# Performance work log

Hardware: AMD Instinct MI355X
Metric: run time of the kernel (lower is better)

The kernel has to match this reference:

```python
import jax, jax.numpy as jnp
import numpy as np

DIM = 384
HEADS = 8
SR = 2
EPS = 1e-5


def setup_inputs() -> dict:
    key = jax.random.key(0)
    ks = jax.random.split(key, 10)
    B, H, W, C = 16, 56, 56, DIM
    s = 0.02
    return {
        "x": jax.random.normal(ks[0], (B, H * W, C), jnp.float32),
        "qkv_w": jax.random.normal(ks[1], (3 * C, C), jnp.float32) * s,
        "qkv_b": jnp.zeros((3 * C,), jnp.float32),
        "proj_w": jax.random.normal(ks[2], (C, C), jnp.float32) * s,
        "proj_b": jnp.zeros((C,), jnp.float32),
        "lp_w": jax.random.normal(ks[3], (C, SR, SR), jnp.float32) * s,  # depthwise convT weight (C,1,sr,sr) squeezed
        "lp_b": jnp.zeros((C,), jnp.float32),
        "ln_w": jnp.ones((C,), jnp.float32),
        "ln_b": jnp.zeros((C,), jnp.float32),
        "H": 56,
        "W": 56,
    }


def reference(x, qkv_w, qkv_b, proj_w, proj_b, lp_w, lp_b, ln_w, ln_b, H, W):
    B, N, C = x.shape
    hd = C // HEADS
    scale = hd ** -0.5

    # AvgPool2d(kernel=(1,1), stride=(sr,sr)) == strided subsampling
    xi = x.transpose(0, 2, 1).reshape(B, C, H, W)[:, :, ::SR, ::SR]
    h, w = H // SR, W // SR
    n = h * w
    xs = xi.reshape(B, C, n).transpose(0, 2, 1)  # [B, n, C]

    qkv = (xs @ qkv_w.T + qkv_b).reshape(B, n, 3, HEADS, hd).transpose(2, 0, 3, 1, 4)
    q, k, v = qkv[0], qkv[1], qkv[2]  # each [B, heads, n, hd]

    attn = jax.nn.softmax(jnp.einsum('bhqd,bhkd->bhqk', q, k) * scale, axis=-1)
    o = jnp.einsum('bhqk,bhkd->bhqd', attn, v).transpose(0, 2, 1, 3).reshape(B, n, C)

    # ConvTranspose2d(C, C, kernel=sr, stride=sr, groups=C): each input pixel
    # expands to an sr x sr block scaled by the per-channel kernel.
    oi = o.transpose(0, 2, 1).reshape(B, C, h, w)
    up = jnp.einsum('bchw,cpq->bchpwq', oi, lp_w).reshape(B, C, H, W)
    up = up + lp_b[None, :, None, None]

    y = up.reshape(B, C, N).transpose(0, 2, 1)  # [B, N, C]
    mu = y.mean(-1, keepdims=True)
    var = y.var(-1, keepdims=True)
    y = (y - mu) * jax.lax.rsqrt(var + EPS) * ln_w + ln_b

    return y @ proj_w.T + proj_b
```

## Files before the change

### kernel.cpp

```cpp
#include <hip/hip_runtime.h>
#include <math.h>

#define CDIM 384
#define NHEADS 8
#define HD 48
#define NQ 784
#define NQPAD 832
#define NB 16
#define HWD 56
#define NPIX 3136
#define QK_SCALE (0.14433756729740643f * 1.4426950408889634f)
#define LN_EPS 1e-5f
#define WSCALE 16.0f
#define WUNSCALE 0.0625f

typedef _Float16 f16;
typedef _Float16 f16x4 __attribute__((ext_vector_type(4)));
typedef _Float16 f16x8 __attribute__((ext_vector_type(8)));
typedef float f32x4 __attribute__((ext_vector_type(4)));

__device__ __forceinline__ float waveSum(float v) {
#pragma unroll
  for (int o = 32; o > 0; o >>= 1) v += __shfl_xor(v, o);
  return v;
}

__device__ __forceinline__ float fast_exp2(float x) {
#if __has_builtin(__builtin_amdgcn_exp2f)
  return __builtin_amdgcn_exp2f(x);
#else
  return __expf(x * 0.6931471805599453f);
#endif
}

__device__ __forceinline__ void gload16(const void* g, void* l) {
  __builtin_amdgcn_global_load_lds(
      (const __attribute__((address_space(1))) void*)g,
      (__attribute__((address_space(3))) void*)l, 16, 0, 0);
}

__device__ __forceinline__ int xcd_chunk_lin(int b, int nwg) {
  const int c = b & 7, s = b >> 3;
  const int q = nwg >> 3, r = nwg & 7;
  const int off = (c < r) ? c * (q + 1) : r * (q + 1) + (c - r) * q;
  return off + s;
}

__global__ __launch_bounds__(256) void prep_kernel(
    const float* __restrict__ x, f16* __restrict__ xp,
    const float* __restrict__ qkv_w, f16* __restrict__ qkv_wh,
    f16* __restrict__ vt, const float* __restrict__ pw,
    const float* __restrict__ lpw, const float* __restrict__ lnw,
    const float* __restrict__ lp_b, const float* __restrict__ ln_b,
    const float* __restrict__ pb, f16* __restrict__ wq,
    float* __restrict__ cvec) {
  const int blk = blockIdx.x, t = threadIdx.x;
  if (blk < 4704) {
    const int i = (blk * 256 + t) * 4;
    const int row = i / CDIM, col = i % CDIM;
    const int b = row / NQ, qi = row % NQ;
    const int hi = qi / 28, wi = qi % 28;
    const float4 v =
        *(const float4*)(x + ((size_t)(b * NPIX + hi * 112 + wi * 2)) * CDIM + col);
    f16x4 h;
    h.x = (f16)v.x; h.y = (f16)v.y; h.z = (f16)v.z; h.w = (f16)v.w;
    *(f16x4*)(xp + i) = h;
  } else if (blk < 5136) {
    const int i = ((blk - 4704) * 256 + t) * 4;
    const float4 v = *(const float4*)(qkv_w + i);
    f16x4 h;
    h.x = (f16)v.x; h.y = (f16)v.y; h.z = (f16)v.z; h.w = (f16)v.w;
    *(f16x4*)(qkv_wh + i) = h;
  } else if (blk < 5280) {
    const int idx = (blk - 5136) * 256 + t;
    const int row = idx / 6, off = idx % 6;
    float4* p = (float4*)vt + (size_t)row * 104 + 98 + off;
    *p = make_float4(0.f, 0.f, 0.f, 0.f);
  } else if (blk < 5856) {
    const int i4 = ((blk - 5280) * 256 + t) * 4;
    const int f = i4 / CDIM, c = i4 % CDIM;
    const int pq = f / CDIM, j = f % CDIM;
    const float4 wv = *(const float4*)(pw + (size_t)j * CDIM + c);
    const float4 ln = *(const float4*)(lnw + c);
    f16x4 h;
    h.x = (f16)(wv.x * lpw[(c + 0) * 4 + pq] * ln.x * WSCALE);
    h.y = (f16)(wv.y * lpw[(c + 1) * 4 + pq] * ln.y * WSCALE);
    h.z = (f16)(wv.z * lpw[(c + 2) * 4 + pq] * ln.z * WSCALE);
    h.w = (f16)(wv.w * lpw[(c + 3) * 4 + pq] * ln.w * WSCALE);
    *(f16x4*)(wq + i4) = h;
  } else {
    const int j = (blk - 5856) * 4 + (t >> 6);
    const int lane = t & 63;
    float a1 = 0.f, a2 = 0.f, a3 = 0.f;
#pragma unroll
    for (int i = 0; i < 6; ++i) {
      const int c = lane + i * 64;
      const float wv = pw[(size_t)j * CDIM + c];
      a1 += lp_b[c] * lnw[c] * wv;
      a2 += lnw[c] * wv;
      a3 += ln_b[c] * wv;
    }
    a1 = waveSum(a1);
    a2 = waveSum(a2);
    a3 = waveSum(a3);
    if (lane == 0) {
      cvec[j] = a1;
      cvec[CDIM + j] = a2;
      cvec[2 * CDIM + j] = a3 + pb[j];
    }
  }
}

__device__ __forceinline__ void mfma_tile_gemm_db(
    const f16* __restrict__ A, const f16* __restrict__ B, int m0, int n0,
    int K, f32x4 (&acc)[4][4], f16* As, f16* Bs) {
  const int t = threadIdx.x;
  const int lane = t & 63, w = t >> 6;
  const int wm = w >> 1, wn = w & 1;
  const int l15 = lane & 15, l4 = lane >> 4;
  const int rowS = t >> 2;
  const int kb = (t & 3) * 16;
  char* AsB = (char*)As;
  char* BsB = (char*)Bs;
  const char* Ag = (const char*)A + ((size_t)(m0 + rowS) * K) * 2 + kb;
  const char* Bg = (const char*)B + ((size_t)(n0 + rowS) * K) * 2 + kb;
  const size_t row64 = (size_t)64 * K * 2;

  gload16(Ag, AsB + t * 16);
  gload16(Ag + row64, AsB + 4096 + t * 16);
  gload16(Bg, BsB + t * 16);
  gload16(Bg + row64, BsB + 4096 + t * 16);

  int cur = 0;
  for (int k0 = 0; k0 < K; k0 += 32) {
    __syncthreads();
    if (k0 + 32 < K) {
      const int nb_ = cur ^ 1;
      const char* Ag2 = Ag + (size_t)(k0 + 32) * 2;
      const char* Bg2 = Bg + (size_t)(k0 + 32) * 2;
      gload16(Ag2, AsB + nb_ * 8192 + t * 16);
      gload16(Ag2 + row64, AsB + nb_ * 8192 + 4096 + t * 16);
      gload16(Bg2, BsB + nb_ * 8192 + t * 16);
      gload16(Bg2 + row64, BsB + nb_ * 8192 + 4096 + t * 16);
    }
    const char* Ab = AsB + cur * 8192;
    const char* Bb = BsB + cur * 8192;
    f16x8 af[4], bf[4];
#pragma unroll
    for (int i = 0; i < 4; ++i)
      af[i] = *(const f16x8*)(Ab + ((wm * 64 + i * 16 + l15) * 64 + l4 * 16));
#pragma unroll
    for (int j = 0; j < 4; ++j)
      bf[j] = *(const f16x8*)(Bb + ((wn * 64 + j * 16 + l15) * 64 + l4 * 16));
#pragma unroll
    for (int i = 0; i < 4; ++i)
#pragma unroll
      for (int j = 0; j < 4; ++j)
        acc[i][j] =
            __builtin_amdgcn_mfma_f32_16x16x32_f16(af[i], bf[j], acc[i][j], 0, 0, 0);
    cur ^= 1;
  }
}

__global__ __launch_bounds__(256) void qkv_mfma_kernel(
    const f16* __restrict__ xp, const f16* __restrict__ wh,
    const float* __restrict__ qkv_b, f16* __restrict__ qh,
    f16* __restrict__ kh, f16* __restrict__ vt) {
  __shared__ union SU {
    struct { f16 As[2 * 128 * 32]; f16 Bs[2 * 128 * 32]; } s;
    f16 Tr[128][136];
  } u;
  const int lin = xcd_chunk_lin(blockIdx.x, 882);
  const int m0 = (lin / 9) * 128, n0 = (lin % 9) * 128;
  f32x4 acc[4][4] = {};
  mfma_tile_gemm_db(xp, wh, m0, n0, CDIM, acc, u.s.As, u.s.Bs);

  const int t = threadIdx.x, lane = t & 63, w = t >> 6;
  const int wm = w >> 1, wn = w & 1;
  const int l15 = lane & 15, l4 = lane >> 4;
  const int sec = n0 / CDIM;
  const float scl = (sec == 0) ? QK_SCALE : 1.f;

  __syncthreads();

  if (sec < 2) {
#pragma unroll
    for (int j = 0; j < 4; ++j) {
      const int fl_ = wn * 64 + j * 16 + l15;
      const float bias = qkv_b[n0 + fl_];
#pragma unroll
      for (int i = 0; i < 4; ++i)
#pragma unroll
        for (int r = 0; r < 4; ++r)
          u.Tr[wm * 64 + i * 16 + l4 * 4 + r][fl_] =
              (f16)((acc[i][j][r] + bias) * scl);
    }
  } else {
#pragma unroll
    for (int j = 0; j < 4; ++j) {
      const int fl_ = wn * 64 + j * 16 + l15;
      const float bias = qkv_b[n0 + fl_];
#pragma unroll
      for (int i = 0; i < 4; ++i)
#pragma unroll
        for (int r = 0; r < 4; ++r)
          u.Tr[fl_][wm * 64 + i * 16 + l4 * 4 + r] = (f16)(acc[i][j][r] + bias);
    }
  }
  __syncthreads();

#pragma unroll
  for (int c = 0; c < 8; ++c) {
    const int v = c * 256 + t;
    const int rr = v >> 4, u16 = v & 15;
    if (sec < 2) {
      const int qi_l = rr, f_l = u16 * 8;
      const int fr = n0 + f_l - sec * CDIM;
      const int hh = fr / HD, d = fr - hh * HD;
      const int mm = m0 + qi_l, b = mm / NQ, tok = mm - b * NQ;
      f16* dst = (sec == 0 ? qh : kh) +
                 ((size_t)(b * NHEADS + hh) * NQ + tok) * HD + d;
      *(f16x8*)dst = *(const f16x8*)&u.Tr[qi_l][f_l];
    } else {
      const int f_l = rr, qi0 = u16 * 8;
      const int fr = n0 + f_l - 2 * CDIM;
      const int hh = fr / HD, d = fr - hh * HD;
      const int mm = m0 + qi0, b = mm / NQ, tok = mm - b * NQ;
      f16* dst = vt + ((size_t)(b * NHEADS + hh) * HD + d) * NQPAD + tok;
      *(f16x8*)dst = *(const f16x8*)&u.Tr[f_l][qi0];
    }
  }
}

__global__ __launch_bounds__(256) void flash_kernel(
    const f16* __restrict__ qh, const f16* __restrict__ kh,
    const f16* __restrict__ vt, f16* __restrict__ o16) {
  __shared__ f16 PQ[128 * 72];
  __shared__ f16 Ks[64][64];
  __shared__ f16 Vts[48][64];

  f16 (*Qs)[72] = (f16(*)[72])PQ;
  f16 (*Ps)[32][68] = (f16(*)[32][68])PQ;

  const int t = threadIdx.x;
  const int lane = t & 63, w = t >> 6;
  const int quad = lane >> 4, l15 = lane & 15;
  const int q0 = blockIdx.x * 128;
  const int bh = blockIdx.y;

  const f16* qg = qh + (size_t)bh * NQ * HD;
  const f16* kg = kh + (size_t)bh * NQ * HD;
  const f16* vg = vt + (size_t)bh * HD * NQPAD;

  {
    const f16x8 z8 = {};
    *(f16x8*)&Qs[t >> 1][48 + (t & 1) * 8] = z8;
    if (t < 128) {
      const int row = t >> 1, zc = 6 + (t & 1);
      *(f16x8*)&Ks[row][(zc ^ (row & 7)) * 8] = z8;
    }
  }

#pragma unroll
  for (int c = 0; c < 3; ++c) {
    const int u = t + c * 256;
    const int row = u / 6, seg = u % 6;
    const int gr = min(q0 + row, NQ - 1);
    *(f16x8*)&Qs[row][seg * 8] =
        *(const f16x8*)(qg + (size_t)gr * HD + seg * 8);
  }
  __syncthreads();

  f16x8 qf0[2], qf1[2];
#pragma unroll
  for (int qa = 0; qa < 2; ++qa) {
    const int row = w * 32 + qa * 16 + l15;
    qf0[qa] = *(const f16x8*)&Qs[row][quad * 8];
    qf1[qa] = *(const f16x8*)&Qs[row][32 + quad * 8];
  }

  const f16* gp[3];
  f16* lp[3];
  int step[3];
#pragma unroll
  for (int c = 0; c < 3; ++c) {
    const int u = t + c * 256;
    if (u < 384) {
      const int row = u / 6, seg = u % 6;
      gp[c] = kg + (size_t)row * HD + seg * 8;
      lp[c] = &Ks[row][(seg ^ (row & 7)) * 8];
      step[c] = 64 * HD;
    } else {
      const int uv = u - 384;
      const int row = uv >> 3, seg = uv & 7;
      gp[c] = vg + (size_t)row * NQPAD + seg * 8;
      lp[c] = &Vts[row][(seg ^ (row & 7)) * 8];
      step[c] = 64;
    }
  }

  f16x8 rg[3];
#pragma unroll
  for (int c = 0; c < 3; ++c) {
    rg[c] = *(const f16x8*)gp[c];
    gp[c] += step[c];
  }

  f32x4 accO[2][3] = {};
  float l_[2][4] = {};

  for (int kt = 0; kt < 13; ++kt) {
#pragma unroll
    for (int c = 0; c < 3; ++c) *(f16x8*)lp[c] = rg[c];
    __syncthreads();
    if (kt < 12) {
#pragma unroll
      for (int c = 0; c < 3; ++c) {
        rg[c] = *(const f16x8*)gp[c];
        gp[c] += step[c];
      }
    }

    const bool last = (kt == 12);
#pragma unroll
    for (int j = 0; j < 4; ++j) {
      const int krow = j * 16 + l15, ksw = krow & 7;
      const f16x8 b0 = *(const f16x8*)&Ks[krow][(quad ^ ksw) * 8];
      const f16x8 b1 = *(const f16x8*)&Ks[krow][((4 + quad) ^ ksw) * 8];
      f32x4 z0 = {}, z1 = {};
      z0 = __builtin_amdgcn_mfma_f32_16x16x32_f16(qf0[0], b0, z0, 0, 0, 0);
      const f32x4 sj0 = __builtin_amdgcn_mfma_f32_16x16x32_f16(qf1[0], b1, z0, 0, 0, 0);
      z1 = __builtin_amdgcn_mfma_f32_16x16x32_f16(qf0[1], b0, z1, 0, 0, 0);
      const f32x4 sj1 = __builtin_amdgcn_mfma_f32_16x16x32_f16(qf1[1], b1, z1, 0, 0, 0);
      const bool msk = last && (j >= 1);
#pragma unroll
      for (int r = 0; r < 4; ++r) {
        const float p0 = msk ? 0.f : fast_exp2(sj0[r]);
        const float p1 = msk ? 0.f : fast_exp2(sj1[r]);
        l_[0][r] += p0;
        l_[1][r] += p1;
        Ps[w][quad * 4 + r][j * 16 + l15] = (f16)p0;
        Ps[w][16 + quad * 4 + r][j * 16 + l15] = (f16)p1;
      }
    }

    f16x8 ap0[2], ap1[2];
#pragma unroll
    for (int qa = 0; qa < 2; ++qa) {
      const int row = qa * 16 + l15;
      const f16x4 a0 = *(const f16x4*)&Ps[w][row][quad * 8];
      const f16x4 a1 = *(const f16x4*)&Ps[w][row][quad * 8 + 4];
      const f16x4 a2 = *(const f16x4*)&Ps[w][row][32 + quad * 8];
      const f16x4 a3 = *(const f16x4*)&Ps[w][row][32 + quad * 8 + 4];
      ap0[qa] = __builtin_shufflevector(a0, a1, 0, 1, 2, 3, 4, 5, 6, 7);
      ap1[qa] = __builtin_shufflevector(a2, a3, 0, 1, 2, 3, 4, 5, 6, 7);
    }

#pragma unroll
    for (int jn = 0; jn < 3; ++jn) {
      const int vrow = jn * 16 + l15, vsw = vrow & 7;
      const f16x8 v0 = *(const f16x8*)&Vts[vrow][(quad ^ vsw) * 8];
      const f16x8 v1 = *(const f16x8*)&Vts[vrow][((4 + quad) ^ vsw) * 8];
#pragma unroll
      for (int qa = 0; qa < 2; ++qa) {
        accO[qa][jn] =
            __builtin_amdgcn_mfma_f32_16x16x32_f16(ap0[qa], v0, accO[qa][jn], 0, 0, 0);
        accO[qa][jn] =
            __builtin_amdgcn_mfma_f32_16x16x32_f16(ap1[qa], v1, accO[qa][jn], 0, 0, 0);
      }
    }
    __syncthreads();
  }

  const int b = bh >> 3, hh = bh & 7;
#pragma unroll
  for (int qa = 0; qa < 2; ++qa) {
#pragma unroll
    for (int r = 0; r < 4; ++r) {
      float rs = l_[qa][r];
      rs += __shfl_xor(rs, 1);
      rs += __shfl_xor(rs, 2);
      rs += __shfl_xor(rs, 4);
      rs += __shfl_xor(rs, 8);
      const int qrow = q0 + w * 32 + qa * 16 + quad * 4 + r;
      if (qrow < NQ) {
        const float inv = 1.f / rs;
#pragma unroll
        for (int jn = 0; jn < 3; ++jn)
          o16[((size_t)(b * NQ + qrow)) * CDIM + hh * HD + jn * 16 + l15] =
              (f16)(accO[qa][jn][r] * inv);
      }
    }
  }
}

__global__ __launch_bounds__(256) void stats_kernel(
    const f16* __restrict__ o16, const float* __restrict__ lp_w,
    const float* __restrict__ lp_b, float* __restrict__ stats) {
  const int m = blockIdx.x * 4 + (threadIdx.x >> 6);
  const int lane = threadIdx.x & 63;
  float s[4] = {}, ss[4] = {};
#pragma unroll
  for (int i = 0; i < 6; ++i) {
    const int c = lane + i * 64;
    const float ov = (float)o16[(size_t)m * CDIM + c];
    const float4 w4 = *(const float4*)(lp_w + c * 4);
    const float bb = lp_b[c];
    const float u0 = ov * w4.x + bb;
    const float u1 = ov * w4.y + bb;
    const float u2 = ov * w4.z + bb;
    const float u3 = ov * w4.w + bb;
    s[0] += u0; ss[0] += u0 * u0;
    s[1] += u1; ss[1] += u1 * u1;
    s[2] += u2; ss[2] += u2 * u2;
    s[3] += u3; ss[3] += u3 * u3;
  }
#pragma unroll
  for (int pq = 0; pq < 4; ++pq) {
    s[pq] = waveSum(s[pq]);
    ss[pq] = waveSum(ss[pq]);
  }
  if (lane < 4) {
    const float mu = s[lane] * (1.f / CDIM);
    const float var = ss[lane] * (1.f / CDIM) - mu * mu;
    stats[m * 8 + lane * 2] = mu;
    stats[m * 8 + lane * 2 + 1] = rsqrtf(var + LN_EPS);
  }
}

__global__ __launch_bounds__(256) void projfused_kernel(
    const f16* __restrict__ o16, const f16* __restrict__ wq,
    const float* __restrict__ stats, const float* __restrict__ cvec,
    float* __restrict__ out) {
  __shared__ f16 As[2 * 128 * 32];
  __shared__ f16 Bs[2 * 128 * 32];
  const int lin = xcd_chunk_lin(blockIdx.x, 1176);
  const int m0 = (lin / 12) * 128, n0 = (lin % 12) * 128;
  f32x4 acc[4][4] = {};
  mfma_tile_gemm_db(o16, wq, m0, n0, CDIM, acc, As, Bs);

  const int t = threadIdx.x, lane = t & 63, w = t >> 6;
  const int wm = w >> 1, wn = w & 1;
  const int l15 = lane & 15, l4 = lane >> 4;
  const int pq = n0 / CDIM;
  const int p = pq >> 1, q = pq & 1;
  const int c0 = n0 - pq * CDIM;

  float C1[4], C2[4], C3[4];
#pragma unroll
  for (int j = 0; j < 4; ++j) {
    const int col = c0 + wn * 64 + j * 16 + l15;
    C1[j] = cvec[col];
    C2[j] = cvec[CDIM + col];
    C3[j] = cvec[2 * CDIM + col];
  }

#pragma unroll
  for (int i = 0; i < 4; ++i) {
#pragma unroll
    for (int r = 0; r < 4; ++r) {
      const int m = m0 + wm * 64 + i * 16 + l4 * 4 + r;
      const int b = m / NQ, n = m % NQ;
      const int hi2 = n / 28, wi2 = n % 28;
      const float mu = stats[m * 8 + pq * 2];
      const float rstd = stats[m * 8 + pq * 2 + 1];
      const int pix = (hi2 * 2 + p) * HWD + (wi2 * 2 + q);
      float* orow = out + ((size_t)(b * NPIX + pix)) * CDIM;
#pragma unroll
      for (int j = 0; j < 4; ++j) {
        const int col = c0 + wn * 64 + j * 16 + l15;
        orow[col] = rstd * (acc[i][j][r] * WUNSCALE + C1[j] - mu * C2[j]) + C3[j];
      }
    }
  }
}

extern "C" void kernel_launch(void* const* d_in, const int* in_sizes, int n_in,
                              void* d_out, int out_size, void* d_ws,
                              size_t ws_size, hipStream_t stream) {
  const float* x      = (const float*)d_in[0];
  const float* qkv_w  = (const float*)d_in[1];
  const float* qkv_b  = (const float*)d_in[2];
  const float* proj_w = (const float*)d_in[3];
  const float* proj_b = (const float*)d_in[4];
  const float* lp_w   = (const float*)d_in[5];
  const float* lp_b   = (const float*)d_in[6];
  const float* ln_w   = (const float*)d_in[7];
  const float* ln_b   = (const float*)d_in[8];
  float* out = (float*)d_out;

  float* ws = (float*)d_ws;
  f16* o16 = (f16*)ws;
  float* zreg = ws + 2408448;
  f16* qh = (f16*)zreg;
  f16* kh = qh + (size_t)128 * NQ * HD;
  f16* vt = kh + (size_t)128 * NQ * HD;
  float* rest = zreg + 7372800;
  f16* xp = (f16*)rest;
  f16* qkv_wh = xp + (size_t)12544 * CDIM;
  float* rest2 = rest + 2408448 + 221184;
  f16* wq = (f16*)rest2;
  float* cvec = rest2 + 1179648;
  float* stats = cvec + 1152;

  prep_kernel<<<dim3(5952), 256, 0, stream>>>(x, xp, qkv_w, qkv_wh, vt, proj_w,
                                              lp_w, ln_w, lp_b, ln_b, proj_b,
                                              wq, cvec);

  qkv_mfma_kernel<<<dim3(882), 256, 0, stream>>>(xp, qkv_wh, qkv_b, qh, kh, vt);

  flash_kernel<<<dim3(7, 128), 256, 0, stream>>>(qh, kh, vt, o16);

  stats_kernel<<<dim3(3136), 256, 0, stream>>>(o16, lp_w, lp_b, stats);

  projfused_kernel<<<dim3(1176), 256, 0, stream>>>(o16, wq, stats, cvec, out);
}
```

Before: 242.8 us.

## Triple-buffer GEMM LDS pipeline with explicit vmcnt waits; pad flash K/V tiles

The shared GEMM mainloop moves from a double-buffered scheme with a full __syncthreads per step to a three-stage LDS ring. Two K-slices are kept in flight, and explicit s_waitcnt vmcnt plus a raw s_barrier replace the full synchronisation, aiming to hide global-load latency behind the MFMA work. K is fixed to CDIM and the loop is fully unrolled. In the flash kernel the XOR-swizzled K/V LDS tiles become row-padded (stride 72) tiles, which simplifies addressing but costs more LDS. The larger LDS footprint in the GEMM kernels may reduce occupancy.

```diff
diff --git a/kernel.cpp b/kernel.cpp
--- a/kernel.cpp
+++ b/kernel.cpp
@@ -111,9 +111,9 @@
   }
 }
 
-__device__ __forceinline__ void mfma_tile_gemm_db(
+__device__ __forceinline__ void mfma_tile_gemm_pipe(
     const f16* __restrict__ A, const f16* __restrict__ B, int m0, int n0,
-    int K, f32x4 (&acc)[4][4], f16* As, f16* Bs) {
+    f32x4 (&acc)[4][4], f16* As, f16* Bs) {
   const int t = threadIdx.x;
   const int lane = t & 63, w = t >> 6;
   const int wm = w >> 1, wn = w & 1;
@@ -122,29 +122,35 @@
   const int kb = (t & 3) * 16;
   char* AsB = (char*)As;
   char* BsB = (char*)Bs;
-  const char* Ag = (const char*)A + ((size_t)(m0 + rowS) * K) * 2 + kb;
-  const char* Bg = (const char*)B + ((size_t)(n0 + rowS) * K) * 2 + kb;
-  const size_t row64 = (size_t)64 * K * 2;
-
-  gload16(Ag, AsB + t * 16);
-  gload16(Ag + row64, AsB + 4096 + t * 16);
-  gload16(Bg, BsB + t * 16);
-  gload16(Bg + row64, BsB + 4096 + t * 16);
-
-  int cur = 0;
-  for (int k0 = 0; k0 < K; k0 += 32) {
-    __syncthreads();
-    if (k0 + 32 < K) {
-      const int nb_ = cur ^ 1;
-      const char* Ag2 = Ag + (size_t)(k0 + 32) * 2;
-      const char* Bg2 = Bg + (size_t)(k0 + 32) * 2;
-      gload16(Ag2, AsB + nb_ * 8192 + t * 16);
-      gload16(Ag2 + row64, AsB + nb_ * 8192 + 4096 + t * 16);
-      gload16(Bg2, BsB + nb_ * 8192 + t * 16);
-      gload16(Bg2 + row64, BsB + nb_ * 8192 + 4096 + t * 16);
-    }
-    const char* Ab = AsB + cur * 8192;
-    const char* Bb = BsB + cur * 8192;
+  const char* Ag = (const char*)A + ((size_t)(m0 + rowS) * CDIM) * 2 + kb;
+  const char* Bg = (const char*)B + ((size_t)(n0 + rowS) * CDIM) * 2 + kb;
+  const size_t row64 = (size_t)64 * CDIM * 2;
+
+#define ISSUE(kk)                                           \
+  do {                                                      \
+    const int bofs = ((kk) % 3) * 8192;                     \
+    const char* Ag2 = Ag + (size_t)(kk) * 64;               \
+    const char* Bg2 = Bg + (size_t)(kk) * 64;               \
+    gload16(Ag2, AsB + bofs + t * 16);                      \
+    gload16(Ag2 + row64, AsB + bofs + 4096 + t * 16);       \
+    gload16(Bg2, BsB + bofs + t * 16);                      \
+    gload16(Bg2 + row64, BsB + bofs + 4096 + t * 16);       \
+  } while (0)
+
+  ISSUE(0);
+  ISSUE(1);
+
+#pragma unroll
+  for (int k = 0; k < 12; ++k) {
+    if (k < 11)
+      asm volatile("s_waitcnt vmcnt(4)" ::: "memory");
+    else
+      asm volatile("s_waitcnt vmcnt(0)" ::: "memory");
+    __builtin_amdgcn_s_barrier();
+    __builtin_amdgcn_sched_barrier(0);
+    if (k + 2 < 12) ISSUE(k + 2);
+    const char* Ab = AsB + (k % 3) * 8192;
+    const char* Bb = BsB + (k % 3) * 8192;
     f16x8 af[4], bf[4];
 #pragma unroll
     for (int i = 0; i < 4; ++i)
@@ -158,8 +164,8 @@
       for (int j = 0; j < 4; ++j)
         acc[i][j] =
             __builtin_amdgcn_mfma_f32_16x16x32_f16(af[i], bf[j], acc[i][j], 0, 0, 0);
-    cur ^= 1;
-  }
+  }
+#undef ISSUE
 }
 
 __global__ __launch_bounds__(256) void qkv_mfma_kernel(
@@ -167,13 +173,13 @@
     const float* __restrict__ qkv_b, f16* __restrict__ qh,
     f16* __restrict__ kh, f16* __restrict__ vt) {
   __shared__ union SU {
-    struct { f16 As[2 * 128 * 32]; f16 Bs[2 * 128 * 32]; } s;
+    struct { f16 As[3 * 128 * 32]; f16 Bs[3 * 128 * 32]; } s;
     f16 Tr[128][136];
   } u;
   const int lin = xcd_chunk_lin(blockIdx.x, 882);
   const int m0 = (lin / 9) * 128, n0 = (lin % 9) * 128;
   f32x4 acc[4][4] = {};
-  mfma_tile_gemm_db(xp, wh, m0, n0, CDIM, acc, u.s.As, u.s.Bs);
+  mfma_tile_gemm_pipe(xp, wh, m0, n0, acc, u.s.As, u.s.Bs);
 
   const int t = threadIdx.x, lane = t & 63, w = t >> 6;
   const int wm = w >> 1, wn = w & 1;
@@ -236,8 +242,8 @@
     const f16* __restrict__ qh, const f16* __restrict__ kh,
     const f16* __restrict__ vt, f16* __restrict__ o16) {
   __shared__ f16 PQ[128 * 72];
-  __shared__ f16 Ks[64][64];
-  __shared__ f16 Vts[48][64];
+  __shared__ f16 Ks[64][72];
+  __shared__ f16 Vts[48][72];
 
   f16 (*Qs)[72] = (f16(*)[72])PQ;
   f16 (*Ps)[32][68] = (f16(*)[32][68])PQ;
@@ -255,10 +261,7 @@
   {
     const f16x8 z8 = {};
     *(f16x8*)&Qs[t >> 1][48 + (t & 1) * 8] = z8;
-    if (t < 128) {
-      const int row = t >> 1, zc = 6 + (t & 1);
-      *(f16x8*)&Ks[row][(zc ^ (row & 7)) * 8] = z8;
-    }
+    if (t < 128) *(f16x8*)&Ks[t >> 1][48 + (t & 1) * 8] = z8;
   }
 
 #pragma unroll
@@ -288,13 +291,13 @@
     if (u < 384) {
       const int row = u / 6, seg = u % 6;
       gp[c] = kg + (size_t)row * HD + seg * 8;
-      lp[c] = &Ks[row][(seg ^ (row & 7)) * 8];
+      lp[c] = &Ks[row][seg * 8];
       step[c] = 64 * HD;
     } else {
       const int uv = u - 384;
       const int row = uv >> 3, seg = uv & 7;
       gp[c] = vg + (size_t)row * NQPAD + seg * 8;
-      lp[c] = &Vts[row][(seg ^ (row & 7)) * 8];
+      lp[c] = &Vts[row][seg * 8];
       step[c] = 64;
     }
   }
@@ -324,9 +327,8 @@
     const bool last = (kt == 12);
 #pragma unroll
     for (int j = 0; j < 4; ++j) {
-      const int krow = j * 16 + l15, ksw = krow & 7;
-      const f16x8 b0 = *(const f16x8*)&Ks[krow][(quad ^ ksw) * 8];
-      const f16x8 b1 = *(const f16x8*)&Ks[krow][((4 + quad) ^ ksw) * 8];
+      const f16x8 b0 = *(const f16x8*)&Ks[j * 16 + l15][quad * 8];
+      const f16x8 b1 = *(const f16x8*)&Ks[j * 16 + l15][32 + quad * 8];
       f32x4 z0 = {}, z1 = {};
       z0 = __builtin_amdgcn_mfma_f32_16x16x32_f16(qf0[0], b0, z0, 0, 0, 0);
       const f32x4 sj0 = __builtin_amdgcn_mfma_f32_16x16x32_f16(qf1[0], b1, z0, 0, 0, 0);
@@ -358,9 +360,8 @@
 
 #pragma unroll
     for (int jn = 0; jn < 3; ++jn) {
-      const int vrow = jn * 16 + l15, vsw = vrow & 7;
-      const f16x8 v0 = *(const f16x8*)&Vts[vrow][(quad ^ vsw) * 8];
-      const f16x8 v1 = *(const f16x8*)&Vts[vrow][((4 + quad) ^ vsw) * 8];
+      const f16x8 v0 = *(const f16x8*)&Vts[jn * 16 + l15][quad * 8];
+      const f16x8 v1 = *(const f16x8*)&Vts[jn * 16 + l15][32 + quad * 8];
 #pragma unroll
       for (int qa = 0; qa < 2; ++qa) {
         accO[qa][jn] =
@@ -432,12 +433,12 @@
     const f16* __restrict__ o16, const f16* __restrict__ wq,
     const float* __restrict__ stats, const float* __restrict__ cvec,
     float* __restrict__ out) {
-  __shared__ f16 As[2 * 128 * 32];
-  __shared__ f16 Bs[2 * 128 * 32];
+  __shared__ f16 As[3 * 128 * 32];
+  __shared__ f16 Bs[3 * 128 * 32];
   const int lin = xcd_chunk_lin(blockIdx.x, 1176);
   const int m0 = (lin / 12) * 128, n0 = (lin % 12) * 128;
   f32x4 acc[4][4] = {};
-  mfma_tile_gemm_db(o16, wq, m0, n0, CDIM, acc, As, Bs);
+  mfma_tile_gemm_pipe(o16, wq, m0, n0, acc, As, Bs);
 
   const int t = threadIdx.x, lane = t & 63, w = t >> 6;
   const int wm = w >> 1, wn = w & 1;
```

Result: no change. 242.2 us (-0.2%).
